# Kernel optimization log

Hardware: AMD Instinct MI355X
Metric: run time of the kernel (lower is better)

## Reference

```python
import jax, jax.numpy as jnp
import numpy as np

B, S, E, H = 2, 2048, 1024, 16
HD = E // H


def setup_inputs() -> dict:
    key = jax.random.key(0)
    ks = jax.random.split(key, 5)
    scale = 0.02
    return {
        "x": jax.random.normal(ks[0], (B, S, E), dtype=jnp.float32),
        "qkv_w": jax.random.normal(ks[1], (3 * E, E), dtype=jnp.float32) * scale,
        "qkv_b": jax.random.normal(ks[2], (3 * E,), dtype=jnp.float32) * scale,
        "out_w": jax.random.normal(ks[3], (E, E), dtype=jnp.float32) * scale,
        "out_b": jax.random.normal(ks[4], (E,), dtype=jnp.float32) * scale,
    }


def reference(x, qkv_w, qkv_b, out_w, out_b):
    b, s, e = x.shape
    scale = 1.0 / jnp.sqrt(jnp.float32(HD))
    # fused QKV projection: torch Linear is x @ W.T + b
    qkv = x @ qkv_w.T + qkv_b                       # [b, s, 3e]
    qkv = qkv.reshape(b, s, 3, H, HD)
    qkv = jnp.transpose(qkv, (2, 0, 3, 1, 4))       # [3, b, h, s, hd]
    q, k, v = qkv[0], qkv[1], qkv[2]
    scores = jnp.einsum('bhqd,bhkd->bhqk', q, k) * scale
    # causal mask (atmask=True): mask strictly upper triangle
    causal = jnp.triu(jnp.ones((s, s), dtype=bool), k=1)
    scores = jnp.where(causal, -jnp.inf, scores)
    attn = jax.nn.softmax(scores, axis=-1)          # dropout p=0.0 -> identity
    out = jnp.einsum('bhqk,bhkd->bhqd', attn, v)    # [b, h, s, hd]
    out = jnp.transpose(out, (0, 2, 1, 3)).reshape(b, s, e)
    return out @ out_w.T + out_b
```

## Files before the change

kernel.cpp:

```cpp
#include <hip/hip_runtime.h>
#include <cmath>

typedef __attribute__((ext_vector_type(8))) __bf16 bf16x8;
typedef __attribute__((ext_vector_type(8))) unsigned short ushort8v;
typedef __attribute__((ext_vector_type(4))) float f32x4;

__device__ inline unsigned short f2bf(float f) {
    unsigned int u = __float_as_uint(f);
    unsigned int r = (u + 0x7fffu + ((u >> 16) & 1u)) >> 16;
    return (unsigned short)r;
}

__device__ inline bf16x8 ld8(const unsigned short* p) {
    uint4 v = *(const uint4*)p;
    return __builtin_bit_cast(bf16x8, v);
}

__device__ inline f32x4 mfma16(bf16x8 a, bf16x8 b, f32x4 c) {
    return __builtin_amdgcn_mfma_f32_16x16x32_bf16(a, b, c, 0, 0, 0);
}

__device__ inline unsigned pk2t(float a, float b) {
    return __builtin_amdgcn_perm(__float_as_uint(b), __float_as_uint(a), 0x07060302u);
}

__device__ inline void gl_lds16(const unsigned short* g, const unsigned short* l) {
    __builtin_amdgcn_global_load_lds(
        (const __attribute__((address_space(1))) void*)(unsigned long long)g,
        (__attribute__((address_space(3))) void*)(unsigned)(unsigned long long)l,
        16, 0, 0);
}

#define NX4  1048576
#define NW14 786432
#define NW24 262144
__global__ __launch_bounds__(256) void cvt3(const float* __restrict__ x,
                                            const float* __restrict__ w1,
                                            const float* __restrict__ w2,
                                            unsigned short* __restrict__ xb,
                                            unsigned short* __restrict__ w1b,
                                            unsigned short* __restrict__ w2b) {
    int i = blockIdx.x * 256 + threadIdx.x;
    const float* src;
    unsigned short* dst;
    int off;
    if (i < NX4)              { src = x;  dst = xb;  off = i; }
    else if (i < NX4 + NW14)  { src = w1; dst = w1b; off = i - NX4; }
    else                      { src = w2; dst = w2b; off = i - NX4 - NW14; }
    float4 v = ((const float4*)src)[off];
    ushort4 o;
    o.x = f2bf(v.x); o.y = f2bf(v.y); o.z = f2bf(v.z); o.w = f2bf(v.w);
    ((ushort4*)dst)[off] = o;
}

__global__ __launch_bounds__(256) void gemm_out(const unsigned short* __restrict__ A,
                                                const unsigned short* __restrict__ B,
                                                const float* __restrict__ bias,
                                                float* __restrict__ C,
                                                int M, int N, int K) {
    __shared__ __align__(16) unsigned short As0[64 * 32];
    __shared__ __align__(16) unsigned short Bs0[128 * 32];
    __shared__ __align__(16) unsigned short As1[64 * 32];
    __shared__ __align__(16) unsigned short Bs1[128 * 32];
    const int m0 = blockIdx.y * 64;
    const int n0 = blockIdx.x * 128;
    const int t = threadIdx.x;
    const int wave = t >> 6, lane = t & 63;
    const int l16 = lane & 15, quad = lane >> 4;
    const int wm = (wave >> 1) * 32, wn = (wave & 1) * 64;

    f32x4 acc[2][4] = {};

    const int ra = t >> 2, ka = (t & 3) * 8;
    const int b1 = 256 + t;
    const int rb0 = t >> 2, kb0 = (t & 3) * 8;
    const int rb1 = b1 >> 2, kb1 = (b1 & 3) * 8;

    for (int k0 = 0; k0 < K; k0 += 64) {
        __syncthreads();
        gl_lds16(A + (size_t)(m0 + ra) * K + k0 + ka,        As0 + t * 8);
        gl_lds16(B + (size_t)(n0 + rb0) * K + k0 + kb0,      Bs0 + t * 8);
        gl_lds16(B + (size_t)(n0 + rb1) * K + k0 + kb1,      Bs0 + b1 * 8);
        gl_lds16(A + (size_t)(m0 + ra) * K + k0 + 32 + ka,   As1 + t * 8);
        gl_lds16(B + (size_t)(n0 + rb0) * K + k0 + 32 + kb0, Bs1 + t * 8);
        gl_lds16(B + (size_t)(n0 + rb1) * K + k0 + 32 + kb1, Bs1 + b1 * 8);
        __syncthreads();

        bf16x8 af[2], bfr[4];
        #pragma unroll
        for (int i = 0; i < 2; ++i)
            af[i] = ld8(As0 + (wm + i * 16 + l16) * 32 + quad * 8);
        #pragma unroll
        for (int j = 0; j < 4; ++j)
            bfr[j] = ld8(Bs0 + (wn + j * 16 + l16) * 32 + quad * 8);
        #pragma unroll
        for (int i = 0; i < 2; ++i)
            #pragma unroll
            for (int j = 0; j < 4; ++j)
                acc[i][j] = mfma16(af[i], bfr[j], acc[i][j]);

        #pragma unroll
        for (int i = 0; i < 2; ++i)
            af[i] = ld8(As1 + (wm + i * 16 + l16) * 32 + quad * 8);
        #pragma unroll
        for (int j = 0; j < 4; ++j)
            bfr[j] = ld8(Bs1 + (wn + j * 16 + l16) * 32 + quad * 8);
        #pragma unroll
        for (int i = 0; i < 2; ++i)
            #pragma unroll
            for (int j = 0; j < 4; ++j)
                acc[i][j] = mfma16(af[i], bfr[j], acc[i][j]);
    }

    #pragma unroll
    for (int i = 0; i < 2; ++i) {
        #pragma unroll
        for (int j = 0; j < 4; ++j) {
            int col = n0 + wn + j * 16 + l16;
            float bv = bias[col];
            #pragma unroll
            for (int r = 0; r < 4; ++r) {
                int row = m0 + wm + i * 16 + quad * 4 + r;
                C[(size_t)row * N + col] = acc[i][j][r] + bv;
            }
        }
    }
}

__global__ __launch_bounds__(256) void gemm_qkv(const unsigned short* __restrict__ A,
                                                const unsigned short* __restrict__ B,
                                                const float* __restrict__ bias,
                                                unsigned short* __restrict__ qp,
                                                unsigned short* __restrict__ kvp,
                                                int M, int N, int K) {
    __shared__ __align__(16) unsigned short Ep[16384];
    unsigned short* As0 = Ep;
    unsigned short* Bs0 = Ep + 4096;
    unsigned short* As1 = Ep + 8192;
    unsigned short* Bs1 = Ep + 12288;
    const int m0 = blockIdx.y * 128;
    const int n0 = blockIdx.x * 128;
    const int t = threadIdx.x;
    const int wave = t >> 6, lane = t & 63;
    const int l16 = lane & 15, quad = lane >> 4;
    const int wm = (wave >> 1) * 64, wn = (wave & 1) * 64;

    f32x4 acc[4][4] = {};

    const int c0 = t, c1 = 256 + t;
    const int r0 = c0 >> 2, kc0 = (c0 & 3) * 8;
    const int r1 = c1 >> 2, kc1 = (c1 & 3) * 8;

    for (int k0 = 0; k0 < K; k0 += 64) {
        __syncthreads();
        gl_lds16(A + (size_t)(m0 + r0) * K + k0 + kc0,      As0 + c0 * 8);
        gl_lds16(B + (size_t)(n0 + r0) * K + k0 + kc0,      Bs0 + c0 * 8);
        gl_lds16(A + (size_t)(m0 + r1) * K + k0 + kc1,      As0 + c1 * 8);
        gl_lds16(B + (size_t)(n0 + r1) * K + k0 + kc1,      Bs0 + c1 * 8);
        gl_lds16(A + (size_t)(m0 + r0) * K + k0 + 32 + kc0, As1 + c0 * 8);
        gl_lds16(B + (size_t)(n0 + r0) * K + k0 + 32 + kc0, Bs1 + c0 * 8);
        gl_lds16(A + (size_t)(m0 + r1) * K + k0 + 32 + kc1, As1 + c1 * 8);
        gl_lds16(B + (size_t)(n0 + r1) * K + k0 + 32 + kc1, Bs1 + c1 * 8);
        __syncthreads();

        bf16x8 af[4], bfr[4];
        #pragma unroll
        for (int i = 0; i < 4; ++i)
            af[i] = ld8(As0 + (wm + i * 16 + l16) * 32 + quad * 8);
        #pragma unroll
        for (int j = 0; j < 4; ++j)
            bfr[j] = ld8(Bs0 + (wn + j * 16 + l16) * 32 + quad * 8);
        #pragma unroll
        for (int i = 0; i < 4; ++i)
            #pragma unroll
            for (int j = 0; j < 4; ++j)
                acc[i][j] = mfma16(af[i], bfr[j], acc[i][j]);

        #pragma unroll
        for (int i = 0; i < 4; ++i)
            af[i] = ld8(As1 + (wm + i * 16 + l16) * 32 + quad * 8);
        #pragma unroll
        for (int j = 0; j < 4; ++j)
            bfr[j] = ld8(Bs1 + (wn + j * 16 + l16) * 32 + quad * 8);
        #pragma unroll
        for (int i = 0; i < 4; ++i)
            #pragma unroll
            for (int j = 0; j < 4; ++j)
                acc[i][j] = mfma16(af[i], bfr[j], acc[i][j]);
    }

    __syncthreads();
    const int b = m0 >> 11;

    if (n0 < 1024) {
        #pragma unroll
        for (int j = 0; j < 4; ++j) {
            int cl = wn + j * 16 + l16;
            float bv = bias[n0 + cl];
            int hrel = cl >> 6, d = cl & 63;
            int half = d >> 5, qd = d & 31;
            int obase = hrel * 8192 + half * 512 + (qd >> 3) * 128 + (qd & 7) + quad * 32;
            #pragma unroll
            for (int i = 0; i < 4; ++i) {
                int ob = obase + ((wm + i * 16) >> 4) * 1024;
                #pragma unroll
                for (int r = 0; r < 4; ++r)
                    Ep[ob + r * 8] = f2bf((acc[i][j][r] + bv) * 0.180336880f);
            }
        }
        __syncthreads();
        const int h0 = n0 >> 6, qt0 = (m0 & 2047) >> 4;
        #pragma unroll
        for (int k = 0; k < 8; ++k) {
            int u = t + 256 * k;
            int cq = u >> 7, within = u & 127;
            int bh = b * 16 + h0 + (cq >> 3);
            int qt = qt0 + (cq & 7);
            *(uint4*)(qp + (size_t)(bh * 128 + qt) * 1024 + within * 8) =
                *(const uint4*)(Ep + u * 8);
        }
    } else if (n0 < 2048) {
        const int f2 = (quad & 1) * 2, krow = quad >> 1;
        #pragma unroll
        for (int j = 0; j < 4; ++j) {
            int cl = wn + j * 16 + l16;
            float bv = bias[n0 + cl];
            int hrel = cl >> 6, d = cl & 63;
            int fbit0 = d >> 5, qd = d & 31;
            int obase = hrel * 8192 + (f2 | fbit0) * 512 + (qd >> 3) * 128 +
                        krow * 32 + (qd & 7);
            #pragma unroll
            for (int i = 0; i < 4; ++i) {
                int ob = obase + ((wm + i * 16) >> 5) * 2048 + (i & 1) * 64;
                #pragma unroll
                for (int r = 0; r < 4; ++r)
                    Ep[ob + r * 8] = f2bf(acc[i][j][r] + bv);
            }
        }
        __syncthreads();
        const int h0 = (n0 - 1024) >> 6, tile0 = (m0 & 2047) >> 5;
        #pragma unroll
        for (int k = 0; k < 8; ++k) {
            int u = t + 256 * k;
            int ck = u >> 8, within = u & 255;
            int bh = b * 16 + h0 + (ck >> 2);
            int tile = tile0 + (ck & 3);
            *(uint4*)(kvp + (size_t)(bh * 64 + tile) * 4096 + within * 8) =
                *(const uint4*)(Ep + u * 8);
        }
    } else {
        const int krow = quad >> 1, e4 = (quad & 1) * 4;
        #pragma unroll
        for (int j = 0; j < 4; ++j) {
            int cl = wn + j * 16 + l16;
            float bv = bias[n0 + cl];
            int hrel = cl >> 6, d = cl & 63;
            int tn = d >> 4, l16v = d & 15;
            int obase = hrel * 8192 + tn * 512 + (krow * 16 + l16v) * 8 + e4;
            #pragma unroll
            for (int i = 0; i < 4; ++i) {
                int ob = obase + ((wm + i * 16) >> 5) * 2048 + (i & 1) * 256;
                unsigned short tmp[4];
                #pragma unroll
                for (int r = 0; r < 4; ++r) tmp[r] = f2bf(acc[i][j][r] + bv);
                *(unsigned long long*)(Ep + ob) = *(const unsigned long long*)tmp;
            }
        }
        __syncthreads();
        const int h0 = (n0 - 2048) >> 6, tile0 = (m0 & 2047) >> 5;
        #pragma unroll
        for (int k = 0; k < 8; ++k) {
            int u = t + 256 * k;
            int ck = u >> 8, within = u & 255;
            int bh = b * 16 + h0 + (ck >> 2);
            int tile = tile0 + (ck & 3);
            *(uint4*)(kvp + (size_t)(bh * 64 + tile) * 4096 + 2048 + within * 8) =
                *(const uint4*)(Ep + u * 8);
        }
    }
}

__global__ __launch_bounds__(256, 3) void attn_kernel(const unsigned short* __restrict__ qp,
                                                      const unsigned short* __restrict__ kvp,
                                                      unsigned short* __restrict__ out) {
    const int S = 2048, E = 1024;
    const int wavei = threadIdx.x >> 6;
    const int lane = threadIdx.x & 63;
    const int l16 = lane & 15, quad = lane >> 4;
    const int bidx = blockIdx.x;
    const int bh = (bidx & 7) * 4 + ((bidx >> 3) & 3);
    const int P = 63 - (bidx >> 5);
    const int b = bh >> 4, h = bh & 15;
    const int loff = lane * 8;

    const unsigned short* qbase = qp + ((size_t)(bh * 128 + 2 * P) * 2) * 512;
    bf16x8 bqA0 = ld8(qbase + loff);
    bf16x8 bqA1 = ld8(qbase + 512 + loff);
    bf16x8 bqB0 = ld8(qbase + 1024 + loff);
    bf16x8 bqB1 = ld8(qbase + 1536 + loff);

    ushort8v ov;
    #pragma unroll
    for (int j = 0; j < 8; ++j) ov[j] = 0x3F80;
    const bf16x8 ones = __builtin_bit_cast(bf16x8, ov);

    f32x4 OA[4] = {}, OB[4] = {};
    f32x4 LA = {}, LB = {};
    const int qA = 32 * P + l16, qB = qA + 16;
    const int nchunks = (P + 2) >> 1;
    const unsigned short* tbase = kvp + (size_t)bh * 64 * 4096;

    for (int c = wavei; c < nchunks; c += 4) {
        const unsigned short* tb = tbase + (size_t)c * 8192;
        bf16x8 f[16];
        #pragma unroll
        for (int i = 0; i < 16; ++i) f[i] = ld8(tb + i * 512 + loff);

        const bool lastc = (c == nchunks - 1);
        const int ks = c * 64;
        const bool skip1 = lastc && ((P & 1) == 0);

        #pragma unroll
        for (int tile = 0; tile < 2; ++tile) {
            if (tile == 1 && skip1) break;
            const bf16x8* g = f + tile * 8;
            const int kst = ks + tile * 32;

            f32x4 sA0 = {}, sA1 = {}, sB0 = {}, sB1 = {};
            sA0 = mfma16(g[0], bqA0, sA0);
            sA0 = mfma16(g[1], bqA1, sA0);
            sA1 = mfma16(g[2], bqA0, sA1);
            sA1 = mfma16(g[3], bqA1, sA1);
            sB0 = mfma16(g[0], bqB0, sB0);
            sB0 = mfma16(g[1], bqB1, sB0);
            sB1 = mfma16(g[2], bqB0, sB1);
            sB1 = mfma16(g[3], bqB1, sB1);

            float pA0[4], pA1[4], pB0[4], pB1[4];
            if (lastc) {
                #pragma unroll
                for (int r = 0; r < 4; ++r) {
                    int kk = kst + quad * 8 + r;
                    pA0[r] = (kk > qA)     ? 0.f : __builtin_amdgcn_exp2f(sA0[r]);
                    pA1[r] = (kk + 4 > qA) ? 0.f : __builtin_amdgcn_exp2f(sA1[r]);
                    pB0[r] = (kk > qB)     ? 0.f : __builtin_amdgcn_exp2f(sB0[r]);
                    pB1[r] = (kk + 4 > qB) ? 0.f : __builtin_amdgcn_exp2f(sB1[r]);
                }
            } else {
                #pragma unroll
                for (int r = 0; r < 4; ++r) {
                    pA0[r] = __builtin_amdgcn_exp2f(sA0[r]);
                    pA1[r] = __builtin_amdgcn_exp2f(sA1[r]);
                    pB0[r] = __builtin_amdgcn_exp2f(sB0[r]);
                    pB1[r] = __builtin_amdgcn_exp2f(sB1[r]);
                }
            }
            uint4 pwA, pwB;
            pwA.x = pk2t(pA0[0], pA0[1]);
            pwA.y = pk2t(pA0[2], pA0[3]);
            pwA.z = pk2t(pA1[0], pA1[1]);
            pwA.w = pk2t(pA1[2], pA1[3]);
            pwB.x = pk2t(pB0[0], pB0[1]);
            pwB.y = pk2t(pB0[2], pB0[3]);
            pwB.z = pk2t(pB1[0], pB1[1]);
            pwB.w = pk2t(pB1[2], pB1[3]);
            bf16x8 bpA = __builtin_bit_cast(bf16x8, pwA);
            bf16x8 bpB = __builtin_bit_cast(bf16x8, pwB);

            OA[0] = mfma16(g[4], bpA, OA[0]);
            OA[1] = mfma16(g[5], bpA, OA[1]);
            OA[2] = mfma16(g[6], bpA, OA[2]);
            OA[3] = mfma16(g[7], bpA, OA[3]);
            LA    = mfma16(ones, bpA, LA);
            OB[0] = mfma16(g[4], bpB, OB[0]);
            OB[1] = mfma16(g[5], bpB, OB[1]);
            OB[2] = mfma16(g[6], bpB, OB[2]);
            OB[3] = mfma16(g[7], bpB, OB[3]);
            LB    = mfma16(ones, bpB, LB);
        }
    }

    __shared__ float Ob[4][32][66];
    __shared__ float Lb[4][32];
    #pragma unroll
    for (int tn = 0; tn < 4; ++tn)
        #pragma unroll
        for (int r = 0; r < 4; ++r) {
            Ob[wavei][l16][tn * 16 + quad * 4 + r]      = OA[tn][r];
            Ob[wavei][16 + l16][tn * 16 + quad * 4 + r] = OB[tn][r];
        }
    if (quad == 0) {
        Lb[wavei][l16]      = LA[0];
        Lb[wavei][16 + l16] = LB[0];
    }
    __syncthreads();

    const int t = threadIdx.x;
    const int qi = t >> 3, hd0 = (t & 7) * 8;
    float ls = Lb[0][qi] + Lb[1][qi] + Lb[2][qi] + Lb[3][qi];
    const float invl = 1.0f / ls;
    unsigned short o[8];
    #pragma unroll
    for (int k = 0; k < 8; ++k) {
        float a = Ob[0][qi][hd0 + k] + Ob[1][qi][hd0 + k] +
                  Ob[2][qi][hd0 + k] + Ob[3][qi][hd0 + k];
        o[k] = f2bf(a * invl);
    }
    *(uint4*)(out + (size_t)(b * S + 32 * P + qi) * E + h * 64 + hd0) = *(uint4*)o;
}

extern "C" void kernel_launch(void* const* d_in, const int* in_sizes, int n_in,
                              void* d_out, int out_size, void* d_ws, size_t ws_size,
                              hipStream_t stream) {
    const float* x     = (const float*)d_in[0];
    const float* qkv_w = (const float*)d_in[1];
    const float* qkv_b = (const float*)d_in[2];
    const float* out_w = (const float*)d_in[3];
    const float* out_b = (const float*)d_in[4];
    float* out = (float*)d_out;

    const int B = 2, S = 2048, E = 1024;
    const int M = B * S;
    const int N1 = 3 * E;

    unsigned short* ws    = (unsigned short*)d_ws;
    unsigned short* xb    = ws;
    unsigned short* w1b   = xb   + (size_t)M * E;
    unsigned short* w2b   = w1b  + (size_t)N1 * E;
    unsigned short* qpb   = w2b  + (size_t)E * E;
    unsigned short* kvpb  = qpb  + (size_t)32 * 128 * 1024;
    unsigned short* attnb = kvpb + (size_t)32 * 64 * 4096;

    cvt3<<<dim3(8192), dim3(256), 0, stream>>>(x, qkv_w, out_w, xb, w1b, w2b);

    gemm_qkv<<<dim3(N1 / 128, M / 128), dim3(256), 0, stream>>>(
        xb, w1b, qkv_b, qpb, kvpb, M, N1, E);

    attn_kernel<<<dim3(2048), dim3(256), 0, stream>>>(qpb, kvpb, attnb);

    gemm_out<<<dim3(E / 128, M / 64), dim3(256), 0, stream>>>(
        attnb, w2b, out_b, out, M, E, E);
}
```

Baseline: 172.4 us.

## Process 64 queries per attention block to double K/V reuse

```diff
diff --git a/kernel.cpp b/kernel.cpp
--- a/kernel.cpp
+++ b/kernel.cpp
@@ -280,7 +280,7 @@
     }
 }
 
-__global__ __launch_bounds__(256, 3) void attn_kernel(const unsigned short* __restrict__ qp,
+__global__ __launch_bounds__(256, 2) void attn_kernel(const unsigned short* __restrict__ qp,
                                                       const unsigned short* __restrict__ kvp,
                                                       unsigned short* __restrict__ out) {
     const int S = 2048, E = 1024;
@@ -289,25 +289,26 @@
     const int l16 = lane & 15, quad = lane >> 4;
     const int bidx = blockIdx.x;
     const int bh = (bidx & 7) * 4 + ((bidx >> 3) & 3);
-    const int P = 63 - (bidx >> 5);
+    const int P = 31 - (bidx >> 5);
     const int b = bh >> 4, h = bh & 15;
     const int loff = lane * 8;
 
-    const unsigned short* qbase = qp + ((size_t)(bh * 128 + 2 * P) * 2) * 512;
-    bf16x8 bqA0 = ld8(qbase + loff);
-    bf16x8 bqA1 = ld8(qbase + 512 + loff);
-    bf16x8 bqB0 = ld8(qbase + 1024 + loff);
-    bf16x8 bqB1 = ld8(qbase + 1536 + loff);
+    const unsigned short* qbase = qp + (size_t)(bh * 128 + 4 * P) * 1024;
+    bf16x8 bq[4][2];
+    #pragma unroll
+    for (int g = 0; g < 4; ++g) {
+        bq[g][0] = ld8(qbase + (2 * g) * 512 + loff);
+        bq[g][1] = ld8(qbase + (2 * g + 1) * 512 + loff);
+    }
 
     ushort8v ov;
     #pragma unroll
     for (int j = 0; j < 8; ++j) ov[j] = 0x3F80;
     const bf16x8 ones = __builtin_bit_cast(bf16x8, ov);
 
-    f32x4 OA[4] = {}, OB[4] = {};
-    f32x4 LA = {}, LB = {};
-    const int qA = 32 * P + l16, qB = qA + 16;
-    const int nchunks = (P + 2) >> 1;
+    f32x4 O[4][4] = {};
+    f32x4 L[4] = {};
+    const int nchunks = P + 1;
     const unsigned short* tbase = kvp + (size_t)bh * 64 * 4096;
 
     for (int c = wavei; c < nchunks; c += 4) {
@@ -318,95 +319,91 @@
 
         const bool lastc = (c == nchunks - 1);
         const int ks = c * 64;
-        const bool skip1 = lastc && ((P & 1) == 0);
 
         #pragma unroll
         for (int tile = 0; tile < 2; ++tile) {
-            if (tile == 1 && skip1) break;
-            const bf16x8* g = f + tile * 8;
+            const bf16x8* g8 = f + tile * 8;
             const int kst = ks + tile * 32;
 
-            f32x4 sA0 = {}, sA1 = {}, sB0 = {}, sB1 = {};
-            sA0 = mfma16(g[0], bqA0, sA0);
-            sA0 = mfma16(g[1], bqA1, sA0);
-            sA1 = mfma16(g[2], bqA0, sA1);
-            sA1 = mfma16(g[3], bqA1, sA1);
-            sB0 = mfma16(g[0], bqB0, sB0);
-            sB0 = mfma16(g[1], bqB1, sB0);
-            sB1 = mfma16(g[2], bqB0, sB1);
-            sB1 = mfma16(g[3], bqB1, sB1);
-
-            float pA0[4], pA1[4], pB0[4], pB1[4];
-            if (lastc) {
-                #pragma unroll
-                for (int r = 0; r < 4; ++r) {
-                    int kk = kst + quad * 8 + r;
-                    pA0[r] = (kk > qA)     ? 0.f : __builtin_amdgcn_exp2f(sA0[r]);
-                    pA1[r] = (kk + 4 > qA) ? 0.f : __builtin_amdgcn_exp2f(sA1[r]);
-                    pB0[r] = (kk > qB)     ? 0.f : __builtin_amdgcn_exp2f(sB0[r]);
-                    pB1[r] = (kk + 4 > qB) ? 0.f : __builtin_amdgcn_exp2f(sB1[r]);
+            f32x4 s0[4], s1[4];
+            #pragma unroll
+            for (int g = 0; g < 4; ++g) { s0[g] = {}; s1[g] = {}; }
+            #pragma unroll
+            for (int g = 0; g < 4; ++g) {
+                s0[g] = mfma16(g8[0], bq[g][0], s0[g]);
+                s0[g] = mfma16(g8[1], bq[g][1], s0[g]);
+                s1[g] = mfma16(g8[2], bq[g][0], s1[g]);
+                s1[g] = mfma16(g8[3], bq[g][1], s1[g]);
+            }
+
+            bf16x8 bp[4];
+            #pragma unroll
+            for (int g = 0; g < 4; ++g) {
+                float p0[4], p1[4];
+                if (lastc) {
+                    const int qg = 64 * P + 16 * g + l16;
+                    #pragma unroll
+                    for (int r = 0; r < 4; ++r) {
+                        int kk = kst + quad * 8 + r;
+                        p0[r] = (kk > qg)     ? 0.f : __builtin_amdgcn_exp2f(s0[g][r]);
+                        p1[r] = (kk + 4 > qg) ? 0.f : __builtin_amdgcn_exp2f(s1[g][r]);
+                    }
+                } else {
+                    #pragma unroll
+                    for (int r = 0; r < 4; ++r) {
+                        p0[r] = __builtin_amdgcn_exp2f(s0[g][r]);
+                        p1[r] = __builtin_amdgcn_exp2f(s1[g][r]);
+                    }
                 }
-            } else {
-                #pragma unroll
-                for (int r = 0; r < 4; ++r) {
-                    pA0[r] = __builtin_amdgcn_exp2f(sA0[r]);
-                    pA1[r] = __builtin_amdgcn_exp2f(sA1[r]);
-                    pB0[r] = __builtin_amdgcn_exp2f(sB0[r]);
-                    pB1[r] = __builtin_amdgcn_exp2f(sB1[r]);
-                }
-            }
-            uint4 pwA, pwB;
-            pwA.x = pk2t(pA0[0], pA0[1]);
-            pwA.y = pk2t(pA0[2], pA0[3]);
-            pwA.z = pk2t(pA1[0], pA1[1]);
-            pwA.w = pk2t(pA1[2], pA1[3]);
-            pwB.x = pk2t(pB0[0], pB0[1]);
-            pwB.y = pk2t(pB0[2], pB0[3]);
-            pwB.z = pk2t(pB1[0], pB1[1]);
-            pwB.w = pk2t(pB1[2], pB1[3]);
-            bf16x8 bpA = __builtin_bit_cast(bf16x8, pwA);
-            bf16x8 bpB = __builtin_bit_cast(bf16x8, pwB);
-
-            OA[0] = mfma16(g[4], bpA, OA[0]);
-            OA[1] = mfma16(g[5], bpA, OA[1]);
-            OA[2] = mfma16(g[6], bpA, OA[2]);
-            OA[3] = mfma16(g[7], bpA, OA[3]);
-            LA    = mfma16(ones, bpA, LA);
-            OB[0] = mfma16(g[4], bpB, OB[0]);
-            OB[1] = mfma16(g[5], bpB, OB[1]);
-            OB[2] = mfma16(g[6], bpB, OB[2]);
-            OB[3] = mfma16(g[7], bpB, OB[3]);
-            LB    = mfma16(ones, bpB, LB);
-        }
-    }
-
-    __shared__ float Ob[4][32][66];
-    __shared__ float Lb[4][32];
+                uint4 pw;
+                pw.x = pk2t(p0[0], p0[1]);
+                pw.y = pk2t(p0[2], p0[3]);
+                pw.z = pk2t(p1[0], p1[1]);
+                pw.w = pk2t(p1[2], p1[3]);
+                bp[g] = __builtin_bit_cast(bf16x8, pw);
+            }
+
+            #pragma unroll
+            for (int g = 0; g < 4; ++g) {
+                O[g][0] = mfma16(g8[4], bp[g], O[g][0]);
+                O[g][1] = mfma16(g8[5], bp[g], O[g][1]);
+                O[g][2] = mfma16(g8[6], bp[g], O[g][2]);
+                O[g][3] = mfma16(g8[7], bp[g], O[g][3]);
+                L[g]    = mfma16(ones, bp[g], L[g]);
+            }
+        }
+    }
+
+    __shared__ float Ob[4][64][66];
+    __shared__ float Lb[4][64];
     #pragma unroll
-    for (int tn = 0; tn < 4; ++tn)
-        #pragma unroll
-        for (int r = 0; r < 4; ++r) {
-            Ob[wavei][l16][tn * 16 + quad * 4 + r]      = OA[tn][r];
-            Ob[wavei][16 + l16][tn * 16 + quad * 4 + r] = OB[tn][r];
-        }
-    if (quad == 0) {
-        Lb[wavei][l16]      = LA[0];
-        Lb[wavei][16 + l16] = LB[0];
+    for (int g = 0; g < 4; ++g) {
+        #pragma unroll
+        for (int tn = 0; tn < 4; ++tn)
+            #pragma unroll
+            for (int r = 0; r < 4; ++r)
+                Ob[wavei][g * 16 + l16][tn * 16 + quad * 4 + r] = O[g][tn][r];
+        if (quad == 0) Lb[wavei][g * 16 + l16] = L[g][0];
     }
     __syncthreads();
 
     const int t = threadIdx.x;
-    const int qi = t >> 3, hd0 = (t & 7) * 8;
+    const int qi = t >> 2, hg = (t & 3) * 16;
     float ls = Lb[0][qi] + Lb[1][qi] + Lb[2][qi] + Lb[3][qi];
     const float invl = 1.0f / ls;
-    unsigned short o[8];
+    const size_t obase = (size_t)(b * S + 64 * P + qi) * E + h * 64;
     #pragma unroll
-    for (int k = 0; k < 8; ++k) {
-        float a = Ob[0][qi][hd0 + k] + Ob[1][qi][hd0 + k] +
-                  Ob[2][qi][hd0 + k] + Ob[3][qi][hd0 + k];
-        o[k] = f2bf(a * invl);
-    }
-    *(uint4*)(out + (size_t)(b * S + 32 * P + qi) * E + h * 64 + hd0) = *(uint4*)o;
+    for (int part = 0; part < 2; ++part) {
+        int hd0 = hg + part * 8;
+        unsigned short o[8];
+        #pragma unroll
+        for (int k = 0; k < 8; ++k) {
+            float a = Ob[0][qi][hd0 + k] + Ob[1][qi][hd0 + k] +
+                      Ob[2][qi][hd0 + k] + Ob[3][qi][hd0 + k];
+            o[k] = f2bf(a * invl);
+        }
+        *(uint4*)(out + obase + hd0) = *(uint4*)o;
+    }
 }
 
 extern "C" void kernel_launch(void* const* d_in, const int* in_sizes, int n_in,
@@ -436,7 +433,7 @@
     gemm_qkv<<<dim3(N1 / 128, M / 128), dim3(256), 0, stream>>>(
         xb, w1b, qkv_b, qpb, kvpb, M, N1, E);
 
-    attn_kernel<<<dim3(2048), dim3(256), 0, stream>>>(qpb, kvpb, attnb);
+    attn_kernel<<<dim3(1024), dim3(256), 0, stream>>>(qpb, kvpb, attnb);
 
     gemm_out<<<dim3(E / 128, M / 64), dim3(256), 0, stream>>>(
         attnb, w2b, out_b, out, M, E, E);
```

Result: no change. 171.5 us (-0.5%).
